# Optimization experiments

Hardware: AMD Instinct MI355X
Metric: run time of the kernel (lower is better)

## Reference

```python
import jax, jax.numpy as jnp
import numpy as np

EMBED_DIM = 1024
NUM_HEADS = 16
D_K = EMBED_DIM // NUM_HEADS
SCALE = D_K ** -0.5
WEIGHT_EPS = 1e-5


def setup_inputs() -> dict:
    key = jax.random.key(0)
    ks = jax.random.split(key, 12)
    B, T, E = 4, 1024, EMBED_DIM
    init = 1.0 / np.sqrt(E)  # ~ nn.Linear default scale
    inp = {
        "q": jax.random.normal(ks[0], (B, T, E), jnp.float32),
        "k": jax.random.normal(ks[1], (B, T, E), jnp.float32),
        "v": jax.random.normal(ks[2], (B, T, E), jnp.float32),
        "weights": jax.random.uniform(ks[3], (B, T), jnp.float32),
        "Wq": jax.random.uniform(ks[4], (E, E), jnp.float32, -init, init),
        "bq": jax.random.uniform(ks[5], (E,), jnp.float32, -init, init),
        "Wk": jax.random.uniform(ks[6], (E, E), jnp.float32, -init, init),
        "bk": jax.random.uniform(ks[7], (E,), jnp.float32, -init, init),
        "Wv": jax.random.uniform(ks[8], (E, E), jnp.float32, -init, init),
        "bv": jax.random.uniform(ks[9], (E,), jnp.float32, -init, init),
        "Wo": jax.random.uniform(ks[10], (E, E), jnp.float32, -init, init),
        "bo": jax.random.uniform(ks[11], (E,), jnp.float32, -init, init),
    }
    return inp


def reference(q, k, v, weights, Wq, bq, Wk, bk, Wv, bv, Wo, bo):
    B, T, E = q.shape
    H, Dk = NUM_HEADS, D_K
    # linear projections (torch Linear: x @ W.T + b), split into heads
    qh = (q @ Wq.T + bq).reshape(B, T, H, Dk).transpose(0, 2, 1, 3)  # [B,H,T,Dk]
    kh = (k @ Wk.T + bk).reshape(B, T, H, Dk).transpose(0, 2, 1, 3)
    vh = (v @ Wv.T + bv).reshape(B, T, H, Dk).transpose(0, 2, 1, 3)
    # scaled energy [B,H,Tq,Tk]
    energy = jnp.einsum("bhqd,bhkd->bhqk", qh, kh) * SCALE
    # weight^2 gating over key axis + masked_fill(-inf) where weight < eps
    w = weights[:, None, None, :]  # [B,1,1,Tk]
    energy = jnp.where(w < WEIGHT_EPS, -jnp.inf, energy * (w * w))
    attn = jax.nn.softmax(energy, axis=-1)  # dropout is identity in eval mode
    out = jnp.einsum("bhqk,bhkd->bhqd", attn, vh)  # [B,H,T,Dk]
    out = out.transpose(0, 2, 1, 3).reshape(B, T, E)
    return out @ Wo.T + bo
```

## Files before the change

kernel.cpp:

```cpp
#include <hip/hip_runtime.h>
#include <hip/hip_bf16.h>
#include <stdint.h>

using frag = __attribute__((ext_vector_type(8))) short;
using f4   = __attribute__((ext_vector_type(4))) float;
using bf16 = __hip_bfloat16;

static constexpr float WEPS = 1e-5f;
static constexpr float SC2K  = 0.125f * 1.44269504f;
static constexpr float EBIAS = -8.0f * 1.44269504f;

#define AS1(p) ((const __attribute__((address_space(1))) void*)(p))
#define AS3(p) ((__attribute__((address_space(3))) void*)(p))

__device__ __forceinline__ void gl2lds16(const void* g, void* l) {
    __builtin_amdgcn_global_load_lds(AS1(g), AS3(l), 16, 0, 0);
}

__device__ inline uint4 pack8(float4 a, float4 b) {
    union { bf16 h[8]; uint4 u; } x;
    x.h[0] = __float2bfloat16(a.x); x.h[1] = __float2bfloat16(a.y);
    x.h[2] = __float2bfloat16(a.z); x.h[3] = __float2bfloat16(a.w);
    x.h[4] = __float2bfloat16(b.x); x.h[5] = __float2bfloat16(b.y);
    x.h[6] = __float2bfloat16(b.z); x.h[7] = __float2bfloat16(b.w);
    return x.u;
}

__device__ __forceinline__ uint2 pack4(float a, float b, float c, float d) {
    union { bf16 h[4]; uint2 u; } x;
    x.h[0] = __float2bfloat16(a); x.h[1] = __float2bfloat16(b);
    x.h[2] = __float2bfloat16(c); x.h[3] = __float2bfloat16(d);
    return x.u;
}

__device__ __forceinline__ int tperm(int t) {
    return (t & ~63) | (((t & 15) << 2) | ((t >> 4) & 3));
}

struct CvtArgs {
    const float* src[7];
    long long    bounds[8];
    long long    total;
};

__global__ __launch_bounds__(256) void cvt_kernel(CvtArgs a, bf16* __restrict__ dst)
{
    long long e = ((long long)blockIdx.x * 256 + threadIdx.x) * 8;
    if (e >= a.total) return;
    int s = 0;
    while (e >= a.bounds[s + 1]) s++;
    const float* src = a.src[s] + (e - a.bounds[s]);
    float4 f0 = ((const float4*)src)[0];
    float4 f1 = ((const float4*)src)[1];
    *(uint4*)(dst + e) = pack8(f0, f1);
}

struct GemmBatch {
    const void*  A[3];
    const void*  W[3];
    const float* bias[3];
    void*        Out[3];
    int          mode[3];
};

template<bool ABF, bool WBF>
__global__ __launch_bounds__(256) void gemm_batch(GemmBatch g)
{
    constexpr int K = 1024;
    __shared__ bf16 As[2][128 * 32];
    __shared__ bf16 Bs[2][128 * 32];

    const int z = blockIdx.z;
    const void*  Ap   = g.A[z];
    const void*  Wp   = g.W[z];
    const float* bias = g.bias[z];
    void*        OutP = g.Out[z];
    const int    mode = g.mode[z];

    const int tid = threadIdx.x;
    const int lid = blockIdx.x + 8 * blockIdx.y;
    const int big   = (lid & 7) * 4 + (lid >> 6);
    const int small = (lid >> 3) & 7;
    int m0, n0;
    if (mode == 4) { m0 = small * 128; n0 = big * 128; }
    else           { m0 = big * 128;   n0 = small * 128; }

    const int lane = tid & 63;
    const int wave = tid >> 6;
    const int wm   = (wave >> 1) * 64;
    const int wn   = (wave & 1) * 64;
    const int lr   = lane & 15;
    const int q    = lane >> 4;

    const int sr = tid >> 1;
    const int sc = (tid & 1) * 16;

    const int c0 = wave * 128 + lane;
    const int c1 = c0 + 64;
    const int r0 = c0 >> 2, col0 = (c0 & 3) * 8;
    const int r1 = c1 >> 2, col1 = (c1 & 3) * 8;

    auto stage = [&](int k0, int pb) {
        if (WBF) {
            const bf16* W = (const bf16*)Wp;
            gl2lds16(&W[(size_t)(n0 + r0) * K + k0 + col0], &Bs[pb][wave * 1024]);
            gl2lds16(&W[(size_t)(n0 + r1) * K + k0 + col1], &Bs[pb][wave * 1024 + 512]);
        } else {
            const float* W = (const float*)Wp;
            const float* src = &W[(size_t)(n0 + sr) * K + k0 + sc];
            float4 f0 = ((const float4*)src)[0];
            float4 f1 = ((const float4*)src)[1];
            float4 f2 = ((const float4*)src)[2];
            float4 f3 = ((const float4*)src)[3];
            *(uint4*)(&Bs[pb][sr * 32 + sc])     = pack8(f0, f1);
            *(uint4*)(&Bs[pb][sr * 32 + sc + 8]) = pack8(f2, f3);
        }
        if (ABF) {
            const bf16* A = (const bf16*)Ap;
            gl2lds16(&A[(size_t)(m0 + r0) * K + k0 + col0], &As[pb][wave * 1024]);
            gl2lds16(&A[(size_t)(m0 + r1) * K + k0 + col1], &As[pb][wave * 1024 + 512]);
        } else {
            const float* A = (const float*)Ap;
            const float* src = &A[(size_t)(m0 + sr) * K + k0 + sc];
            float4 f0 = ((const float4*)src)[0];
            float4 f1 = ((const float4*)src)[1];
            float4 f2 = ((const float4*)src)[2];
            float4 f3 = ((const float4*)src)[3];
            *(uint4*)(&As[pb][sr * 32 + sc])     = pack8(f0, f1);
            *(uint4*)(&As[pb][sr * 32 + sc + 8]) = pack8(f2, f3);
        }
    };

    f4 acc[4][4];
    #pragma unroll
    for (int i = 0; i < 4; i++)
        #pragma unroll
        for (int j = 0; j < 4; j++) acc[i][j] = f4{0.f, 0.f, 0.f, 0.f};

    stage(0, 0);
    __syncthreads();

    for (int kt = 0; kt < 32; kt++) {
        const int cb = kt & 1;
        if (kt < 31) stage((kt + 1) * 32, cb ^ 1);

        frag af[4], bfr[4];
        #pragma unroll
        for (int i = 0; i < 4; i++)
            af[i] = *(const frag*)(&As[cb][(wm + i * 16 + lr) * 32 + q * 8]);
        #pragma unroll
        for (int j = 0; j < 4; j++)
            bfr[j] = *(const frag*)(&Bs[cb][(wn + j * 16 + lr) * 32 + q * 8]);
        #pragma unroll
        for (int i = 0; i < 4; i++)
            #pragma unroll
            for (int j = 0; j < 4; j++)
                acc[i][j] = __builtin_amdgcn_mfma_f32_16x16x32_bf16(af[i], bfr[j], acc[i][j], 0, 0, 0);
        __syncthreads();
    }

    if (mode == 4) {
        const int bbt   = (n0 + wn) >> 10;
        const int tbase = (n0 + wn) & 1023;
        bf16* O = (bf16*)OutP;
        #pragma unroll
        for (int i = 0; i < 4; i++) {
            int row0 = m0 + wm + i * 16 + q * 4;
            #pragma unroll
            for (int r = 0; r < 4; r++) {
                int f = row0 + r;
                int h = f >> 6, d = f & 63;
                float bv = bias[f];
                size_t idx = ((((size_t)bbt * 16 + h) * 64 + d) << 10) + tbase + lr * 4;
                *(uint2*)(&O[idx]) = pack4(acc[i][0][r] + bv, acc[i][1][r] + bv,
                                           acc[i][2][r] + bv, acc[i][3][r] + bv);
            }
        }
    } else {
        #pragma unroll
        for (int i = 0; i < 4; i++) {
            int row0 = m0 + wm + i * 16 + q * 4;
            #pragma unroll
            for (int j = 0; j < 4; j++) {
                int col = n0 + wn + j * 16 + lr;
                float bv = bias[col];
                #pragma unroll
                for (int r = 0; r < 4; r++) {
                    float val = acc[i][j][r] + bv;
                    int mrow = row0 + r;
                    if (mode == 3) {
                        ((float*)OutP)[(size_t)mrow * 1024 + col] = val;
                    } else {
                        int bb = mrow >> 10, t = mrow & 1023;
                        int h  = col >> 6,   d = col & 63;
                        size_t idx;
                        if (mode == 2)
                            idx = ((((size_t)bb * 16 + h) * 64 + d) << 10) + tperm(t);
                        else
                            idx = ((((size_t)bb * 16 + h) << 10) + t) * 64 + d;
                        ((bf16*)OutP)[idx] = __float2bfloat16(val);
                    }
                }
            }
        }
    }
}

template<bool WBF>
__global__ __launch_bounds__(256) void gemm_out(const bf16* __restrict__ A,
                                                const void* __restrict__ Wp,
                                                const float* __restrict__ bias,
                                                float* __restrict__ Out)
{
    constexpr int K = 1024;
    __shared__ bf16 As[3][64 * 64];
    __shared__ bf16 Bs[3][128 * 64];

    const int tid = threadIdx.x;
    const int lid = blockIdx.x + 8 * blockIdx.y;
    const int mt  = (lid & 7) * 8 + (lid >> 6);
    const int nt  = (lid >> 3) & 7;
    const int n0  = nt * 128;
    const int m0  = mt * 64;
    const int lane = tid & 63;
    const int wave = tid >> 6;
    const int wm   = (wave >> 1) * 32;
    const int wn   = (wave & 1) * 64;
    const int lr   = lane & 15;
    const int q    = lane >> 4;

    const int sr = tid >> 1;
    const int sc = (tid & 1) * 32;

    int rb[4], cb4[4];
    #pragma unroll
    for (int gg = 0; gg < 4; gg++) {
        int D = wave * 256 + gg * 64 + lane;
        rb[gg]  = D >> 3;
        cb4[gg] = (D & 7) * 8;
    }
    int ra[2], ca4[2];
    #pragma unroll
    for (int gg = 0; gg < 2; gg++) {
        int D = wave * 128 + gg * 64 + lane;
        ra[gg]  = D >> 3;
        ca4[gg] = (D & 7) * 8;
    }

    auto stage = [&](int k0, int pb) {
        if (WBF) {
            const bf16* W = (const bf16*)Wp;
            #pragma unroll
            for (int gg = 0; gg < 4; gg++)
                gl2lds16(&W[(size_t)(n0 + rb[gg]) * K + k0 + cb4[gg]],
                         &Bs[pb][(wave * 256 + gg * 64) * 8]);
        } else {
            const float* W = (const float*)Wp;
            const float* src = &W[(size_t)(n0 + sr) * K + k0 + sc];
            #pragma unroll
            for (int c = 0; c < 4; c++) {
                float4 f0 = ((const float4*)src)[2 * c];
                float4 f1 = ((const float4*)src)[2 * c + 1];
                *(uint4*)(&Bs[pb][sr * 64 + sc + c * 8]) = pack8(f0, f1);
            }
        }
        #pragma unroll
        for (int gg = 0; gg < 2; gg++)
            gl2lds16(&A[(size_t)(m0 + ra[gg]) * K + k0 + ca4[gg]],
                     &As[pb][(wave * 128 + gg * 64) * 8]);
    };

    f4 acc[2][4];
    #pragma unroll
    for (int i = 0; i < 2; i++)
        #pragma unroll
        for (int j = 0; j < 4; j++) acc[i][j] = f4{0.f, 0.f, 0.f, 0.f};

    stage(0, 0);
    stage(64, 1);
    if (WBF) {
        asm volatile("s_waitcnt vmcnt(6)" ::: "memory");
        __builtin_amdgcn_s_barrier();
    } else {
        __syncthreads();
    }

    int cb = 0;
    for (int kt = 0; kt < 16; kt++) {
        if (kt < 14) {
            int sb = cb + 2; if (sb >= 3) sb -= 3;
            stage((kt + 2) * 64, sb);
        }

        #pragma unroll
        for (int kk = 0; kk < 2; kk++) {
            frag af[2], bfr[4];
            #pragma unroll
            for (int i = 0; i < 2; i++)
                af[i] = *(const frag*)(&As[cb][(wm + i * 16 + lr) * 64 + kk * 32 + q * 8]);
            #pragma unroll
            for (int j = 0; j < 4; j++)
                bfr[j] = *(const frag*)(&Bs[cb][(wn + j * 16 + lr) * 64 + kk * 32 + q * 8]);
            #pragma unroll
            for (int i = 0; i < 2; i++)
                #pragma unroll
                for (int j = 0; j < 4; j++)
                    acc[i][j] = __builtin_amdgcn_mfma_f32_16x16x32_bf16(af[i], bfr[j], acc[i][j], 0, 0, 0);
        }

        if (kt < 15) {
            if (WBF) {
                if (kt < 14) asm volatile("s_waitcnt vmcnt(6)" ::: "memory");
                else         asm volatile("s_waitcnt vmcnt(0)" ::: "memory");
                __builtin_amdgcn_s_barrier();
            } else {
                __syncthreads();
            }
        }
        cb = cb + 1; if (cb == 3) cb = 0;
    }

    #pragma unroll
    for (int i = 0; i < 2; i++) {
        int row0 = m0 + wm + i * 16 + q * 4;
        #pragma unroll
        for (int j = 0; j < 4; j++) {
            int col = n0 + wn + j * 16 + lr;
            float bv = bias[col];
            #pragma unroll
            for (int r = 0; r < 4; r++)
                Out[(size_t)(row0 + r) * 1024 + col] = acc[i][j][r] + bv;
        }
    }
}

__global__ __launch_bounds__(256, 3) void attn_kernel(const bf16* __restrict__ qh,
                                                      const bf16* __restrict__ kh,
                                                      const bf16* __restrict__ vhT,
                                                      const float* __restrict__ wts,
                                                      bf16* __restrict__ att)
{
    constexpr int LDP = 72;
    __shared__ bf16 Ks[2][64 * 64];
    __shared__ bf16 Vs[2][64 * 64];
    __shared__ bf16 Plds[4][32 * LDP];

    const int tid  = threadIdx.x;
    const int lane = tid & 63;
    const int wave = tid >> 6;
    const int lr   = lane & 15;
    const int q    = lane >> 4;
    const int bh   = blockIdx.x;
    const int bb   = bh >> 4;
    const int h    = bh & 15;
    const int q0w  = blockIdx.y * 128 + wave * 32;
    const size_t base = (size_t)bh * 1024 * 64;

    const int cA = wave * 128 + lane;
    const int cB = cA + 64;
    const int rowA = cA >> 3, gA = ((cA & 7) ^ (rowA & 7)) * 8;
    const int rowB = cB >> 3, gB = ((cB & 7) ^ (rowB & 7)) * 8;

    frag aq[2][2];
    #pragma unroll
    for (int rf = 0; rf < 2; rf++)
        #pragma unroll
        for (int ks = 0; ks < 2; ks++)
            aq[rf][ks] = *(const frag*)(&qh[base + (size_t)(q0w + rf * 16 + lr) * 64 + ks * 32 + q * 8]);

    float rs[2][4];
    f4 o[2][4];
    #pragma unroll
    for (int rf = 0; rf < 2; rf++)
        #pragma unroll
        for (int j = 0; j < 4; j++) {
            o[rf][j] = f4{0.f, 0.f, 0.f, 0.f};
            rs[rf][j] = 0.f;
        }

    gl2lds16(&kh [base + (size_t)rowA * 64 + gA],   &Ks[0][wave * 1024]);
    gl2lds16(&kh [base + (size_t)rowB * 64 + gB],   &Ks[0][wave * 1024 + 512]);
    gl2lds16(&vhT[base + (size_t)rowA * 1024 + gA], &Vs[0][wave * 1024]);
    gl2lds16(&vhT[base + (size_t)rowB * 1024 + gB], &Vs[0][wave * 1024 + 512]);
    __syncthreads();

    for (int t = 0; t < 16; t++) {
        const int k0  = t * 64;
        const int buf = t & 1;
        if (t < 15) {
            int kn = k0 + 64;
            gl2lds16(&kh [base + (size_t)(kn + rowA) * 64 + gA],  &Ks[buf ^ 1][wave * 1024]);
            gl2lds16(&kh [base + (size_t)(kn + rowB) * 64 + gB],  &Ks[buf ^ 1][wave * 1024 + 512]);
            gl2lds16(&vhT[base + (size_t)rowA * 1024 + kn + gA], &Vs[buf ^ 1][wave * 1024]);
            gl2lds16(&vhT[base + (size_t)rowB * 1024 + kn + gB], &Vs[buf ^ 1][wave * 1024 + 512]);
        }

        float sc2[4], eb[4];
        #pragma unroll
        for (int j = 0; j < 4; j++) {
            float w = wts[bb * 1024 + k0 + j * 16 + lr];
            sc2[j] = SC2K * w * w;
            eb[j]  = (w < WEPS) ? -1e30f : EBIAS;
        }

        frag kb[4][2];
        #pragma unroll
        for (int j = 0; j < 4; j++) {
            int rowj = j * 16 + lr;
            kb[j][0] = *(const frag*)(&Ks[buf][rowj * 64 + (((q    ) ^ (rowj & 7)) * 8)]);
            kb[j][1] = *(const frag*)(&Ks[buf][rowj * 64 + (((q + 4) ^ (rowj & 7)) * 8)]);
        }

        #pragma unroll
        for (int rf = 0; rf < 2; rf++) {
            f4 s[4];
            #pragma unroll
            for (int j = 0; j < 4; j++) {
                f4 z = f4{0.f, 0.f, 0.f, 0.f};
                s[j] = __builtin_amdgcn_mfma_f32_16x16x32_bf16(aq[rf][0], kb[j][0], z, 0, 0, 0);
                s[j] = __builtin_amdgcn_mfma_f32_16x16x32_bf16(aq[rf][1], kb[j][1], s[j], 0, 0, 0);
            }
            float p[4][4];
            #pragma unroll
            for (int j = 0; j < 4; j++)
                #pragma unroll
                for (int r = 0; r < 4; r++) {
                    p[j][r] = __builtin_amdgcn_exp2f(fmaf(s[j][r], sc2[j], eb[j]));
                    rs[rf][r] += p[j][r];
                }
            #pragma unroll
            for (int r = 0; r < 4; r++)
                *(uint2*)(&Plds[wave][(rf * 16 + q * 4 + r) * LDP + lr * 4]) =
                    pack4(p[0][r], p[1][r], p[2][r], p[3][r]);
        }

        frag vb[4][2];
        #pragma unroll
        for (int j = 0; j < 4; j++) {
            int rowj = j * 16 + lr;
            vb[j][0] = *(const frag*)(&Vs[buf][rowj * 64 + (((q    ) ^ (rowj & 7)) * 8)]);
            vb[j][1] = *(const frag*)(&Vs[buf][rowj * 64 + (((q + 4) ^ (rowj & 7)) * 8)]);
        }

        #pragma unroll
        for (int rf = 0; rf < 2; rf++) {
            frag ap0 = *(const frag*)(&Plds[wave][(rf * 16 + lr) * LDP + q * 8]);
            frag ap1 = *(const frag*)(&Plds[wave][(rf * 16 + lr) * LDP + 32 + q * 8]);
            #pragma unroll
            for (int j = 0; j < 4; j++) {
                o[rf][j] = __builtin_amdgcn_mfma_f32_16x16x32_bf16(ap0, vb[j][0], o[rf][j], 0, 0, 0);
                o[rf][j] = __builtin_amdgcn_mfma_f32_16x16x32_bf16(ap1, vb[j][1], o[rf][j], 0, 0, 0);
            }
        }
        __syncthreads();
    }

    #pragma unroll
    for (int off = 1; off < 16; off <<= 1)
        #pragma unroll
        for (int rf = 0; rf < 2; rf++)
            #pragma unroll
            for (int r = 0; r < 4; r++)
                rs[rf][r] += __shfl_xor(rs[rf][r], off, 64);

    #pragma unroll
    for (int rf = 0; rf < 2; rf++) {
        float inv[4];
        #pragma unroll
        for (int r = 0; r < 4; r++) inv[r] = 1.0f / rs[rf][r];
        const int t0 = q0w + rf * 16 + q * 4;
        #pragma unroll
        for (int j = 0; j < 4; j++) {
            int d = h * 64 + j * 16 + lr;
            #pragma unroll
            for (int r = 0; r < 4; r++)
                att[((size_t)bb * 1024 + t0 + r) * 1024 + d] =
                    __float2bfloat16(o[rf][j][r] * inv[r]);
        }
    }
}

extern "C" void kernel_launch(void* const* d_in, const int* in_sizes, int n_in,
                              void* d_out, int out_size, void* d_ws, size_t ws_size,
                              hipStream_t stream)
{
    const float* q   = (const float*)d_in[0];
    const float* k   = (const float*)d_in[1];
    const float* v   = (const float*)d_in[2];
    const float* wts = (const float*)d_in[3];
    const float* Wq  = (const float*)d_in[4];
    const float* bq  = (const float*)d_in[5];
    const float* Wk  = (const float*)d_in[6];
    const float* bk  = (const float*)d_in[7];
    const float* Wv  = (const float*)d_in[8];
    const float* bv  = (const float*)d_in[9];
    const float* Wo  = (const float*)d_in[10];
    const float* bo  = (const float*)d_in[11];
    float* out = (float*)d_out;

    const long long Mi = 1024 * 1024;
    bf16* qh  = (bf16*)d_ws;
    bf16* kh  = qh  + 4 * Mi;
    bf16* vhT = kh  + 4 * Mi;
    bf16* att = vhT + 4 * Mi;
    bf16* cvt = att + 4 * Mi;
    const size_t base_bytes = (size_t)32 * Mi;

    dim3 blk(256);

    if (ws_size >= base_bytes + (size_t)32 * Mi) {
        CvtArgs ca{};
        ca.src[0] = q;  ca.src[1] = k;  ca.src[2] = v;
        ca.src[3] = Wq; ca.src[4] = Wk; ca.src[5] = Wv; ca.src[6] = Wo;
        long long bnd[8] = {0, 4*Mi, 8*Mi, 12*Mi, 13*Mi, 14*Mi, 15*Mi, 16*Mi};
        for (int i = 0; i < 8; i++) ca.bounds[i] = bnd[i];
        ca.total = 16 * Mi;
        cvt_kernel<<<8192, blk, 0, stream>>>(ca, cvt);

        GemmBatch gq{};
        gq.A[0] = cvt;          gq.A[1] = cvt + 4*Mi;   gq.A[2] = cvt + 14*Mi;
        gq.W[0] = cvt + 12*Mi;  gq.W[1] = cvt + 13*Mi;  gq.W[2] = cvt + 8*Mi;
        gq.bias[0] = bq; gq.bias[1] = bk; gq.bias[2] = bv;
        gq.Out[0] = qh;  gq.Out[1] = kh;  gq.Out[2] = vhT;
        gq.mode[0] = 0;  gq.mode[1] = 0;  gq.mode[2] = 4;
        gemm_batch<true, true><<<dim3(8, 32, 3), blk, 0, stream>>>(gq);

        attn_kernel<<<dim3(64, 8), blk, 0, stream>>>(qh, kh, vhT, wts, att);

        gemm_out<true><<<dim3(8, 64), blk, 0, stream>>>(att, cvt + 15*Mi, bo, out);
    } else if (ws_size >= base_bytes + (size_t)8 * Mi) {
        CvtArgs ca{};
        ca.src[0] = Wq; ca.src[1] = Wk; ca.src[2] = Wv; ca.src[3] = Wo;
        long long bnd[8] = {0, 1*Mi, 2*Mi, 3*Mi, 4*Mi, 4*Mi, 4*Mi, 4*Mi};
        for (int i = 0; i < 8; i++) ca.bounds[i] = bnd[i];
        ca.total = 4 * Mi;
        cvt_kernel<<<2048, blk, 0, stream>>>(ca, cvt);

        GemmBatch gq{};
        gq.A[0] = q; gq.A[1] = k; gq.A[2] = v;
        gq.W[0] = cvt; gq.W[1] = cvt + 1*Mi; gq.W[2] = cvt + 2*Mi;
        gq.bias[0] = bq; gq.bias[1] = bk; gq.bias[2] = bv;
        gq.Out[0] = qh;  gq.Out[1] = kh;  gq.Out[2] = vhT;
        gq.mode[0] = 0;  gq.mode[1] = 0;  gq.mode[2] = 2;
        gemm_batch<false, true><<<dim3(8, 32, 3), blk, 0, stream>>>(gq);

        attn_kernel<<<dim3(64, 8), blk, 0, stream>>>(qh, kh, vhT, wts, att);

        gemm_out<true><<<dim3(8, 64), blk, 0, stream>>>(att, cvt + 3*Mi, bo, out);
    } else {
        GemmBatch gq{};
        gq.A[0] = q; gq.A[1] = k; gq.A[2] = v;
        gq.W[0] = Wq; gq.W[1] = Wk; gq.W[2] = Wv;
        gq.bias[0] = bq; gq.bias[1] = bk; gq.bias[2] = bv;
        gq.Out[0] = qh;  gq.Out[1] = kh;  gq.Out[2] = vhT;
        gq.mode[0] = 0;  gq.mode[1] = 0;  gq.mode[2] = 2;
        gemm_batch<false, false><<<dim3(8, 32, 3), blk, 0, stream>>>(gq);

        attn_kernel<<<dim3(64, 8), blk, 0, stream>>>(qh, kh, vhT, wts, att);

        gemm_out<false><<<dim3(8, 64), blk, 0, stream>>>(att, Wo, bo, out);
    }
}
```

Before: 209.7 us.

## Triple-buffer GEMM LDS staging with partial vmcnt waits for async loads

Replaces the double-buffered LDS pipeline in the batched projection GEMM with a three-stage ring buffer, prefetching two K-tiles ahead. For the bf16 path it waits only for the older global-to-LDS loads using s_waitcnt vmcnt(4) before a raw barrier, instead of a full __syncthreads that drains every outstanding load. This is meant to hide more global load latency, at the cost of 50% more LDS per block, which may reduce occupancy.

```diff
diff --git a/kernel.cpp b/kernel.cpp
--- a/kernel.cpp
+++ b/kernel.cpp
@@ -67,8 +67,8 @@
 __global__ __launch_bounds__(256) void gemm_batch(GemmBatch g)
 {
     constexpr int K = 1024;
-    __shared__ bf16 As[2][128 * 32];
-    __shared__ bf16 Bs[2][128 * 32];
+    __shared__ bf16 As0[128 * 32], As1[128 * 32], As2[128 * 32];
+    __shared__ bf16 Bs0[128 * 32], Bs1[128 * 32], Bs2[128 * 32];
 
     const int z = blockIdx.z;
     const void*  Ap   = g.A[z];
@@ -100,11 +100,11 @@
     const int r0 = c0 >> 2, col0 = (c0 & 3) * 8;
     const int r1 = c1 >> 2, col1 = (c1 & 3) * 8;
 
-    auto stage = [&](int k0, int pb) {
+    auto stage = [&](int k0, bf16* Asd, bf16* Bsd) {
         if (WBF) {
             const bf16* W = (const bf16*)Wp;
-            gl2lds16(&W[(size_t)(n0 + r0) * K + k0 + col0], &Bs[pb][wave * 1024]);
-            gl2lds16(&W[(size_t)(n0 + r1) * K + k0 + col1], &Bs[pb][wave * 1024 + 512]);
+            gl2lds16(&W[(size_t)(n0 + r0) * K + k0 + col0], &Bsd[wave * 1024]);
+            gl2lds16(&W[(size_t)(n0 + r1) * K + k0 + col1], &Bsd[wave * 1024 + 512]);
         } else {
             const float* W = (const float*)Wp;
             const float* src = &W[(size_t)(n0 + sr) * K + k0 + sc];
@@ -112,13 +112,13 @@
             float4 f1 = ((const float4*)src)[1];
             float4 f2 = ((const float4*)src)[2];
             float4 f3 = ((const float4*)src)[3];
-            *(uint4*)(&Bs[pb][sr * 32 + sc])     = pack8(f0, f1);
-            *(uint4*)(&Bs[pb][sr * 32 + sc + 8]) = pack8(f2, f3);
+            *(uint4*)(&Bsd[sr * 32 + sc])     = pack8(f0, f1);
+            *(uint4*)(&Bsd[sr * 32 + sc + 8]) = pack8(f2, f3);
         }
         if (ABF) {
             const bf16* A = (const bf16*)Ap;
-            gl2lds16(&A[(size_t)(m0 + r0) * K + k0 + col0], &As[pb][wave * 1024]);
-            gl2lds16(&A[(size_t)(m0 + r1) * K + k0 + col1], &As[pb][wave * 1024 + 512]);
+            gl2lds16(&A[(size_t)(m0 + r0) * K + k0 + col0], &Asd[wave * 1024]);
+            gl2lds16(&A[(size_t)(m0 + r1) * K + k0 + col1], &Asd[wave * 1024 + 512]);
         } else {
             const float* A = (const float*)Ap;
             const float* src = &A[(size_t)(m0 + sr) * K + k0 + sc];
@@ -126,8 +126,8 @@
             float4 f1 = ((const float4*)src)[1];
             float4 f2 = ((const float4*)src)[2];
             float4 f3 = ((const float4*)src)[3];
-            *(uint4*)(&As[pb][sr * 32 + sc])     = pack8(f0, f1);
-            *(uint4*)(&As[pb][sr * 32 + sc + 8]) = pack8(f2, f3);
+            *(uint4*)(&Asd[sr * 32 + sc])     = pack8(f0, f1);
+            *(uint4*)(&Asd[sr * 32 + sc + 8]) = pack8(f2, f3);
         }
     };
 
@@ -137,26 +137,67 @@
         #pragma unroll
         for (int j = 0; j < 4; j++) acc[i][j] = f4{0.f, 0.f, 0.f, 0.f};
 
-    stage(0, 0);
-    __syncthreads();
-
-    for (int kt = 0; kt < 32; kt++) {
-        const int cb = kt & 1;
-        if (kt < 31) stage((kt + 1) * 32, cb ^ 1);
-
+    auto compute = [&](const bf16* Asp, const bf16* Bsp) {
         frag af[4], bfr[4];
         #pragma unroll
         for (int i = 0; i < 4; i++)
-            af[i] = *(const frag*)(&As[cb][(wm + i * 16 + lr) * 32 + q * 8]);
+            af[i] = *(const frag*)(&Asp[(wm + i * 16 + lr) * 32 + q * 8]);
         #pragma unroll
         for (int j = 0; j < 4; j++)
-            bfr[j] = *(const frag*)(&Bs[cb][(wn + j * 16 + lr) * 32 + q * 8]);
+            bfr[j] = *(const frag*)(&Bsp[(wn + j * 16 + lr) * 32 + q * 8]);
         #pragma unroll
         for (int i = 0; i < 4; i++)
             #pragma unroll
             for (int j = 0; j < 4; j++)
                 acc[i][j] = __builtin_amdgcn_mfma_f32_16x16x32_bf16(af[i], bfr[j], acc[i][j], 0, 0, 0);
+    };
+
+    if (ABF && WBF) {
+        stage(0,  As0, Bs0);
+        stage(32, As1, Bs1);
+        asm volatile("s_waitcnt vmcnt(4)" ::: "memory");
+        __builtin_amdgcn_s_barrier();
+
+        for (int m = 0; m < 10; m++) {
+            const int kb = m * 96;
+            stage(kb + 64, As2, Bs2);
+            compute(As0, Bs0);
+            asm volatile("s_waitcnt vmcnt(4)" ::: "memory");
+            __builtin_amdgcn_s_barrier();
+
+            stage(kb + 96, As0, Bs0);
+            compute(As1, Bs1);
+            asm volatile("s_waitcnt vmcnt(4)" ::: "memory");
+            __builtin_amdgcn_s_barrier();
+
+            stage(kb + 128, As1, Bs1);
+            compute(As2, Bs2);
+            asm volatile("s_waitcnt vmcnt(4)" ::: "memory");
+            __builtin_amdgcn_s_barrier();
+        }
+        compute(As0, Bs0);
+        asm volatile("s_waitcnt vmcnt(0)" ::: "memory");
+        __builtin_amdgcn_s_barrier();
+        compute(As1, Bs1);
+    } else {
+        stage(0,  As0, Bs0);
+        stage(32, As1, Bs1);
         __syncthreads();
+        for (int m = 0; m < 10; m++) {
+            const int kb = m * 96;
+            stage(kb + 64, As2, Bs2);
+            compute(As0, Bs0);
+            __syncthreads();
+            stage(kb + 96, As0, Bs0);
+            compute(As1, Bs1);
+            __syncthreads();
+            stage(kb + 128, As1, Bs1);
+            compute(As2, Bs2);
+            __syncthreads();
+        }
+        compute(As0, Bs0);
+        __syncthreads();
+        compute(As1, Bs1);
     }
 
     if (mode == 4) {
```

Result: no change. 206.8 us (-1.4%).
